# Kernel tuning notes

Hardware: AMD Instinct MI355X
Metric: run time of the kernel (lower is better)

Reference implementation:

```python
import jax, jax.numpy as jnp
import numpy as np

N_TOKENS = 16384
DIM = 1024
E = 8            # num_experts
K = 2            # top-k
CAP_FACTOR = 1.25


def setup_inputs() -> dict:
    key = jax.random.key(0)
    ks = jax.random.split(key, 4)
    sc = 0.02
    return {
        "x": jax.random.normal(ks[0], (N_TOKENS, DIM), jnp.float32),
        "Wr": jax.random.normal(ks[1], (E, DIM), jnp.float32) * sc,
        "br": jnp.zeros((E,), jnp.float32),
        "W1": jax.random.normal(ks[2], (E, DIM, DIM), jnp.float32) * sc,
        "b1": jnp.zeros((E, DIM), jnp.float32),
        "W2": jax.random.normal(ks[3], (E, DIM, DIM), jnp.float32) * sc,
        "b2": jnp.zeros((E, DIM), jnp.float32),
    }


def reference(x, Wr, br, W1, b1, W2, b2):
    N, D = x.shape
    capacity = int(CAP_FACTOR * N / E)  # static python int

    # --- NoisyTopKRouter (eval mode: no noise) ---
    logits = x @ Wr.T + br                                   # [N, E]
    topk_vals, topk_idx = jax.lax.top_k(logits, K)           # [N, K]
    gates_k = jax.nn.softmax(topk_vals, axis=-1)             # [N, K]
    sparse_gates = jnp.zeros_like(logits).at[
        jnp.arange(N)[:, None], topk_idx].set(gates_k)       # [N, E]

    # --- dispatch: first `capacity` tokens (in token order) per expert ---
    mask = sparse_gates > 0                                  # [N, E]
    # stable argsort puts routed tokens first, preserving token order
    order = jnp.argsort(jnp.logical_not(mask), axis=0, stable=True)[:capacity]  # [cap, E]
    valid = jnp.take_along_axis(mask, order, axis=0)         # [cap, E] bool

    tokens = x[order]                                        # [cap, E, D]
    h = jax.nn.relu(jnp.einsum('ced,eod->ceo', tokens, W1) + b1)  # [cap, E, D]
    expert_out = jnp.einsum('ceh,eoh->ceo', h, W2) + b2           # [cap, E, D]

    # --- combine: weight by gate, zero out padding, scatter-add back ---
    w = jnp.take_along_axis(sparse_gates, order, axis=0) * valid.astype(x.dtype)  # [cap, E]
    contrib = expert_out * w[..., None]                      # [cap, E, D]
    output = jnp.zeros_like(x).at[order.reshape(-1)].add(contrib.reshape(-1, D))

    # --- load-balancing stats ---
    load = valid.sum(axis=0).astype(x.dtype)                 # [E]
    load_dist = load / (load.sum() + 1e-8)
    load_loss = -(load_dist * jnp.log(load_dist + 1e-8)).sum()
    return output, load_loss, load_dist
```

## Files before the change

### kernel.cpp

```cpp
#include <hip/hip_runtime.h>
#include <hip/hip_bf16.h>
#include <cstdint>
#include <cstddef>

#define N_TOK   16384
#define DIM     1024
#define NE      8
#define CAP     2560
#define NCHUNK  256
#define NSLOT   (NE * CAP)

#define APL_BYTES  ((size_t)NSLOT * DIM * 2)
#define WPL_BYTES  ((size_t)NE * DIM * DIM * 2)
#define H_BYTES    ((size_t)NSLOT * DIM * 4)
#define TOK_BYTES  ((size_t)NSLOT * 4)
#define GATE_BYTES ((size_t)NSLOT * 4)
#define TIDX_BYTES ((size_t)N_TOK * 2 * 4)
#define TGT_BYTES  ((size_t)N_TOK * 2 * 4)
#define TSLOT_BYTES ((size_t)N_TOK * 2 * 4)
#define CC_BYTES   ((size_t)NE * NCHUNK * 4)
#define CO_BYTES   ((size_t)NE * NCHUNK * 4)
#define SMALL_BYTES (TOK_BYTES + GATE_BYTES + TIDX_BYTES + TGT_BYTES + TSLOT_BYTES + CC_BYTES + CO_BYTES)

typedef __attribute__((ext_vector_type(8))) short short8;
typedef __attribute__((ext_vector_type(4))) short short4v;
typedef __attribute__((ext_vector_type(4))) float floatx4;

__device__ __forceinline__ short f2bf(float f) {
    union { float f; unsigned u; } c; c.f = f;
    unsigned r = (c.u + 0x7fffu + ((c.u >> 16) & 1u)) >> 16;
    return (short)r;
}
__device__ __forceinline__ float bf2f(short s) {
    union { unsigned u; float f; } c; c.u = ((unsigned)(unsigned short)s) << 16;
    return c.f;
}

__device__ __forceinline__ void gload_lds16(const void* g, void* l) {
    typedef const __attribute__((address_space(1))) unsigned int* gp_t;
    typedef __attribute__((address_space(3))) unsigned int* lp_t;
    __builtin_amdgcn_global_load_lds((gp_t)g, (lp_t)l, 16, 0, 0);
}

__global__ __launch_bounds__(256) void router_kernel(
    const float* __restrict__ x, const float* __restrict__ Wr,
    const float* __restrict__ br, int* __restrict__ tokIdx,
    float* __restrict__ tokGate)
{
    int wave = threadIdx.x >> 6;
    int lane = threadIdx.x & 63;
    int t = blockIdx.x * 4 + wave;

    float acc[NE];
#pragma unroll
    for (int e = 0; e < NE; ++e) acc[e] = 0.f;

    const float4* xr = (const float4*)(x + (size_t)t * DIM);
#pragma unroll
    for (int j = 0; j < 4; ++j) {
        float4 xv = xr[j * 64 + lane];
#pragma unroll
        for (int e = 0; e < NE; ++e) {
            float4 wv = ((const float4*)(Wr + e * DIM))[j * 64 + lane];
            acc[e] = fmaf(xv.x, wv.x, acc[e]);
            acc[e] = fmaf(xv.y, wv.y, acc[e]);
            acc[e] = fmaf(xv.z, wv.z, acc[e]);
            acc[e] = fmaf(xv.w, wv.w, acc[e]);
        }
    }
#pragma unroll
    for (int e = 0; e < NE; ++e) {
        float v = acc[e];
#pragma unroll
        for (int off = 32; off > 0; off >>= 1) v += __shfl_xor(v, off, 64);
        acc[e] = v;
    }
    if (lane == 0) {
        float l[NE];
#pragma unroll
        for (int e = 0; e < NE; ++e) l[e] = acc[e] + br[e];
        int i0 = 0; float v0 = l[0];
#pragma unroll
        for (int e = 1; e < NE; ++e) if (l[e] > v0) { v0 = l[e]; i0 = e; }
        int i1 = -1; float v1 = -3.4e38f;
#pragma unroll
        for (int e = 0; e < NE; ++e) if (e != i0 && l[e] > v1) { v1 = l[e]; i1 = e; }
        float e1 = expf(v1 - v0);
        float g0 = 1.f / (1.f + e1);
        float g1 = e1 * g0;
        tokIdx[2 * t] = i0;  tokIdx[2 * t + 1] = i1;
        tokGate[2 * t] = g0; tokGate[2 * t + 1] = g1;
    }
}

__global__ __launch_bounds__(64) void count_kernel(
    const int* __restrict__ tokIdx, int* __restrict__ chunkCounts)
{
    int lane = threadIdx.x;
    int t = blockIdx.x * 64 + lane;
    int i0 = tokIdx[2 * t], i1 = tokIdx[2 * t + 1];
#pragma unroll
    for (int e = 0; e < NE; ++e) {
        unsigned long long m = __ballot(i0 == e || i1 == e);
        if (lane == 0) chunkCounts[e * NCHUNK + blockIdx.x] = __popcll(m);
    }
}

__global__ __launch_bounds__(256) void scan_kernel(
    const int* __restrict__ chunkCounts, int* __restrict__ chunkOffs,
    float* __restrict__ outTail)
{
    __shared__ int s[NCHUNK];
    __shared__ int totals[NE];
    int tid = threadIdx.x;
    for (int e = 0; e < NE; ++e) {
        int v = chunkCounts[e * NCHUNK + tid];
        s[tid] = v;
        __syncthreads();
        for (int off = 1; off < NCHUNK; off <<= 1) {
            int add = (tid >= off) ? s[tid - off] : 0;
            __syncthreads();
            s[tid] += add;
            __syncthreads();
        }
        chunkOffs[e * NCHUNK + tid] = s[tid] - v;
        if (tid == NCHUNK - 1) totals[e] = s[tid];
        __syncthreads();
    }
    if (tid == 0) {
        float load[NE]; float sum = 0.f;
        for (int e = 0; e < NE; ++e) {
            int c = totals[e]; if (c > CAP) c = CAP;
            load[e] = (float)c; sum += load[e];
        }
        float inv = 1.f / (sum + 1e-8f);
        float loss = 0.f;
        for (int e = 0; e < NE; ++e) {
            float d = load[e] * inv;
            loss -= d * logf(d + 1e-8f);
            outTail[1 + e] = d;
        }
        outTail[0] = loss;
    }
}

__global__ __launch_bounds__(64) void emit_kernel(
    const int* __restrict__ tokIdx, const float* __restrict__ tokGate,
    const int* __restrict__ chunkOffs, int* __restrict__ expTok,
    float* __restrict__ expGate, int* __restrict__ tokenSlot)
{
    int lane = threadIdx.x;
    int t = blockIdx.x * 64 + lane;
    int i0 = tokIdx[2 * t], i1 = tokIdx[2 * t + 1];
    float g0 = tokGate[2 * t], g1 = tokGate[2 * t + 1];
#pragma unroll
    for (int e = 0; e < NE; ++e) {
        bool r0 = (i0 == e), r1 = (i1 == e);
        unsigned long long m = __ballot(r0 || r1);
        if (r0 || r1) {
            int rank = chunkOffs[e * NCHUNK + blockIdx.x] +
                       __popcll(m & ((1ull << lane) - 1ull));
            int k = r0 ? 0 : 1;
            if (rank < CAP) {
                expTok[e * CAP + rank] = t;
                expGate[e * CAP + rank] = r0 ? g0 : g1;
                tokenSlot[2 * t + k] = e * CAP + rank;
            } else {
                tokenSlot[2 * t + k] = -1;
            }
        }
    }
}

__global__ __launch_bounds__(256) void convert_kernel(
    const float* __restrict__ src, short* __restrict__ hi,
    short* __restrict__ lo, int n4)
{
    int i = blockIdx.x * 256 + threadIdx.x;
    if (i >= n4) return;
    float4 v = ((const float4*)src)[i];
    short4v h, l;
    h.x = f2bf(v.x); h.y = f2bf(v.y); h.z = f2bf(v.z); h.w = f2bf(v.w);
    l.x = f2bf(v.x - bf2f(h.x)); l.y = f2bf(v.y - bf2f(h.y));
    l.z = f2bf(v.z - bf2f(h.z)); l.w = f2bf(v.w - bf2f(h.w));
    ((short4v*)hi)[i] = h;
    ((short4v*)lo)[i] = l;
}

__global__ __launch_bounds__(256) void gather_kernel(
    const float* __restrict__ x, const int* __restrict__ expTok,
    short* __restrict__ Ahi, short* __restrict__ Alo)
{
    int slot = blockIdx.x;
    int tok = expTok[slot];
    int c = threadIdx.x * 4;
    float4 v = *(const float4*)(x + (size_t)tok * DIM + c);
    short4v h, l;
    h.x = f2bf(v.x); h.y = f2bf(v.y); h.z = f2bf(v.z); h.w = f2bf(v.w);
    l.x = f2bf(v.x - bf2f(h.x)); l.y = f2bf(v.y - bf2f(h.y));
    l.z = f2bf(v.z - bf2f(h.z)); l.w = f2bf(v.w - bf2f(h.w));
    *(short4v*)(Ahi + (size_t)slot * DIM + c) = h;
    *(short4v*)(Alo + (size_t)slot * DIM + c) = l;
}


__device__ __forceinline__ void stage_tile(
    const short* __restrict__ aP, const short* __restrict__ bP,
    int rowBaseA, int rowBaseB, int k0,
    char* ldsA, char* ldsB, int wave, int lane)
{
    const int srow  = lane >> 3;
    const int xcol  = ((lane & 7) ^ srow) * 8;
    const short* ga = aP + (size_t)(rowBaseA + wave * 32 + srow) * DIM + k0 + xcol;
    const short* gb = bP + (size_t)(rowBaseB + wave * 32 + srow) * DIM + k0 + xcol;
    char* la = ldsA + (wave * 32) * 128;
    char* lb = ldsB + (wave * 32) * 128;
#pragma unroll
    for (int g = 0; g < 4; ++g)
        gload_lds16(ga + (size_t)(g * 8) * DIM, la + g * 1024);
#pragma unroll
    for (int g = 0; g < 4; ++g)
        gload_lds16(gb + (size_t)(g * 8) * DIM, lb + g * 1024);
}

template <int MODE>
__global__ __launch_bounds__(256) void mfma_gemm(
    const short* __restrict__ Ahi, const short* __restrict__ Alo,
    const short* __restrict__ Whi, const short* __restrict__ Wlo,
    const float* __restrict__ bias, const float* __restrict__ expGate,
    short* __restrict__ Ohi, short* __restrict__ Olo,
    float* __restrict__ EO)
{
    __shared__ __align__(16) char lds[65536];

    const int flat = blockIdx.x;
    const int swz  = (flat & 7) * 160 + (flat >> 3);
    const int e  = swz / 160;
    const int r  = swz % 160;
    const int tm = r >> 3;
    const int tn = r & 7;

    const int tid  = threadIdx.x;
    const int wave = tid >> 6;
    const int lane = tid & 63;
    const int wm = (wave >> 1) * 64;
    const int wn = (wave & 1) * 64;

    const int rowBaseA = e * CAP + tm * 128;
    const int rowBaseB = tn * 128;
    const short* Wh = Whi + (size_t)e * DIM * DIM;
    const short* Wl = Wlo + (size_t)e * DIM * DIM;

    const int frow = lane & 15;
    const int fq   = lane >> 4;

    floatx4 acc[4][4];
#pragma unroll
    for (int i = 0; i < 4; ++i)
#pragma unroll
        for (int j = 0; j < 4; ++j) acc[i][j] = (floatx4)0.f;

    stage_tile(Ahi, Wh, rowBaseA, rowBaseB, 0, lds, lds + 16384, wave, lane);
    __syncthreads();

#pragma unroll 2
    for (int t = 0; t < 48; ++t) {
        const int p = t & 1;
        char* bufA = lds + p * 32768;
        char* bufB = bufA + 16384;
        if (t < 47) {
            const int t1 = t + 1;
            const int seg = t1 >> 4;
            const int k0  = (t1 & 15) << 6;
            const short* aP = (seg == 2) ? Alo : Ahi;
            const short* bP = (seg == 1) ? Wl : Wh;
            stage_tile(aP, bP, rowBaseA, rowBaseB, k0,
                       lds + (p ^ 1) * 32768, lds + (p ^ 1) * 32768 + 16384,
                       wave, lane);
        }
#pragma unroll
        for (int kc = 0; kc < 2; ++kc) {
            const int bo = ((kc * 4 + fq) ^ (frow & 7)) * 16;
            short8 af[4], bf[4];
#pragma unroll
            for (int i = 0; i < 4; ++i)
                af[i] = *(const short8*)(bufA + (wm + i * 16 + frow) * 128 + bo);
#pragma unroll
            for (int j = 0; j < 4; ++j)
                bf[j] = *(const short8*)(bufB + (wn + j * 16 + frow) * 128 + bo);
            __builtin_amdgcn_s_setprio(1);
#pragma unroll
            for (int i = 0; i < 4; ++i)
#pragma unroll
                for (int j = 0; j < 4; ++j)
                    acc[i][j] = __builtin_amdgcn_mfma_f32_16x16x32_bf16(
                        af[i], bf[j], acc[i][j], 0, 0, 0);
            __builtin_amdgcn_s_setprio(0);
        }
        __syncthreads();
    }

    const int colBase = tn * 128 + wn;
#pragma unroll
    for (int j = 0; j < 4; ++j) {
        const int gc = colBase + j * 16 + (lane & 15);
        const float bj = bias[(size_t)e * DIM + gc];
#pragma unroll
        for (int i = 0; i < 4; ++i) {
            const int lr0 = wm + i * 16 + (lane >> 4) * 4;
#pragma unroll
            for (int rr = 0; rr < 4; ++rr) {
                const int lr = tm * 128 + lr0 + rr;
                float v = acc[i][j][rr] + bj;
                if (MODE == 0) {
                    v = fmaxf(v, 0.f);
                    short hi = f2bf(v);
                    short lo = f2bf(v - bf2f(hi));
                    size_t idx = (size_t)(e * CAP + lr) * DIM + gc;
                    Ohi[idx] = hi;
                    Olo[idx] = lo;
                } else {
                    float g = expGate[e * CAP + lr];
                    EO[(size_t)(e * CAP + lr) * DIM + gc] = v * g;
                }
            }
        }
    }
}

__global__ __launch_bounds__(256) void combine_kernel(
    const float* __restrict__ EO, const int* __restrict__ tokenSlot,
    float* __restrict__ out)
{
    int t = blockIdx.x;
    int col = threadIdx.x * 4;
    int p0 = tokenSlot[2 * t], p1 = tokenSlot[2 * t + 1];
    float4 s = make_float4(0.f, 0.f, 0.f, 0.f);
    if (p0 >= 0) {
        float4 v = *(const float4*)(EO + (size_t)p0 * DIM + col);
        s.x += v.x; s.y += v.y; s.z += v.z; s.w += v.w;
    }
    if (p1 >= 0) {
        float4 v = *(const float4*)(EO + (size_t)p1 * DIM + col);
        s.x += v.x; s.y += v.y; s.z += v.z; s.w += v.w;
    }
    *(float4*)(out + (size_t)t * DIM + col) = s;
}

#define BM 128
#define BN 128
#define BKF 8

__global__ __launch_bounds__(256) void f32gemm1_kernel(
    const float* __restrict__ x, const float* __restrict__ W1,
    const float* __restrict__ b1, const int* __restrict__ expTok,
    float* __restrict__ h)
{
    int e = blockIdx.z;
    int tm = blockIdx.x, tn = blockIdx.y;
    const float* W = W1 + (size_t)e * DIM * DIM;
    __shared__ float As[BKF][BM];
    __shared__ float Bs[BKF][BN];
    int tid = threadIdx.x;
    int lrow = tid >> 1, lk4 = (tid & 1) * 4;
    int rm = tid >> 4, rn = tid & 15;
    int tok = expTok[e * CAP + tm * BM + lrow];
    const float* aPtr = x + (size_t)tok * DIM + lk4;
    const float* bPtr = W + (size_t)(tn * BN + lrow) * DIM + lk4;
    float acc[8][8];
#pragma unroll
    for (int i = 0; i < 8; ++i)
#pragma unroll
        for (int j = 0; j < 8; ++j) acc[i][j] = 0.f;
    for (int k0 = 0; k0 < DIM; k0 += BKF) {
        float4 av = *(const float4*)(aPtr + k0);
        float4 bv = *(const float4*)(bPtr + k0);
        __syncthreads();
        As[lk4 + 0][lrow] = av.x; As[lk4 + 1][lrow] = av.y;
        As[lk4 + 2][lrow] = av.z; As[lk4 + 3][lrow] = av.w;
        Bs[lk4 + 0][lrow] = bv.x; Bs[lk4 + 1][lrow] = bv.y;
        Bs[lk4 + 2][lrow] = bv.z; Bs[lk4 + 3][lrow] = bv.w;
        __syncthreads();
#pragma unroll
        for (int k = 0; k < BKF; ++k) {
            float4 a0 = *(const float4*)&As[k][rm * 4];
            float4 a1 = *(const float4*)&As[k][64 + rm * 4];
            float4 b0 = *(const float4*)&Bs[k][rn * 4];
            float4 b1r = *(const float4*)&Bs[k][64 + rn * 4];
            float ar[8] = {a0.x,a0.y,a0.z,a0.w,a1.x,a1.y,a1.z,a1.w};
            float bc[8] = {b0.x,b0.y,b0.z,b0.w,b1r.x,b1r.y,b1r.z,b1r.w};
#pragma unroll
            for (int i = 0; i < 8; ++i)
#pragma unroll
                for (int j = 0; j < 8; ++j)
                    acc[i][j] = fmaf(ar[i], bc[j], acc[i][j]);
        }
    }
    int o0 = tn * BN + rn * 4;
    float4 blo = *(const float4*)(b1 + e * DIM + o0);
    float4 bhi = *(const float4*)(b1 + e * DIM + o0 + 64);
#pragma unroll
    for (int i = 0; i < 8; ++i) {
        int c = tm * BM + ((i < 4) ? (rm * 4 + i) : (64 + rm * 4 + i - 4));
        float* hr = h + ((size_t)e * CAP + c) * DIM;
        float4 lo = make_float4(fmaxf(acc[i][0] + blo.x, 0.f),
                                fmaxf(acc[i][1] + blo.y, 0.f),
                                fmaxf(acc[i][2] + blo.z, 0.f),
                                fmaxf(acc[i][3] + blo.w, 0.f));
        float4 hi = make_float4(fmaxf(acc[i][4] + bhi.x, 0.f),
                                fmaxf(acc[i][5] + bhi.y, 0.f),
                                fmaxf(acc[i][6] + bhi.z, 0.f),
                                fmaxf(acc[i][7] + bhi.w, 0.f));
        *(float4*)(hr + o0) = lo;
        *(float4*)(hr + o0 + 64) = hi;
    }
}

__global__ __launch_bounds__(256) void f32gemm2_kernel(
    const float* __restrict__ h, const float* __restrict__ W2,
    const float* __restrict__ b2, const int* __restrict__ expTok,
    const float* __restrict__ expGate, float* __restrict__ out)
{
    int e = blockIdx.z;
    int tm = blockIdx.x, tn = blockIdx.y;
    const float* W = W2 + (size_t)e * DIM * DIM;
    __shared__ float As[BKF][BM];
    __shared__ float Bs[BKF][BN];
    int tid = threadIdx.x;
    int lrow = tid >> 1, lk4 = (tid & 1) * 4;
    int rm = tid >> 4, rn = tid & 15;
    const float* aPtr = h + ((size_t)e * CAP + tm * BM + lrow) * DIM + lk4;
    const float* bPtr = W + (size_t)(tn * BN + lrow) * DIM + lk4;
    float acc[8][8];
#pragma unroll
    for (int i = 0; i < 8; ++i)
#pragma unroll
        for (int j = 0; j < 8; ++j) acc[i][j] = 0.f;
    for (int k0 = 0; k0 < DIM; k0 += BKF) {
        float4 av = *(const float4*)(aPtr + k0);
        float4 bv = *(const float4*)(bPtr + k0);
        __syncthreads();
        As[lk4 + 0][lrow] = av.x; As[lk4 + 1][lrow] = av.y;
        As[lk4 + 2][lrow] = av.z; As[lk4 + 3][lrow] = av.w;
        Bs[lk4 + 0][lrow] = bv.x; Bs[lk4 + 1][lrow] = bv.y;
        Bs[lk4 + 2][lrow] = bv.z; Bs[lk4 + 3][lrow] = bv.w;
        __syncthreads();
#pragma unroll
        for (int k = 0; k < BKF; ++k) {
            float4 a0 = *(const float4*)&As[k][rm * 4];
            float4 a1 = *(const float4*)&As[k][64 + rm * 4];
            float4 b0 = *(const float4*)&Bs[k][rn * 4];
            float4 b1r = *(const float4*)&Bs[k][64 + rn * 4];
            float ar[8] = {a0.x,a0.y,a0.z,a0.w,a1.x,a1.y,a1.z,a1.w};
            float bc[8] = {b0.x,b0.y,b0.z,b0.w,b1r.x,b1r.y,b1r.z,b1r.w};
#pragma unroll
            for (int i = 0; i < 8; ++i)
#pragma unroll
                for (int j = 0; j < 8; ++j)
                    acc[i][j] = fmaf(ar[i], bc[j], acc[i][j]);
        }
    }
    int o0 = tn * BN + rn * 4;
    float4 blo = *(const float4*)(b2 + e * DIM + o0);
    float4 bhi = *(const float4*)(b2 + e * DIM + o0 + 64);
#pragma unroll
    for (int i = 0; i < 8; ++i) {
        int c = tm * BM + ((i < 4) ? (rm * 4 + i) : (64 + rm * 4 + i - 4));
        float g = expGate[e * CAP + c];
        if (g != 0.f) {
            int t = expTok[e * CAP + c];
            float* orow = out + (size_t)t * DIM;
            atomicAdd(orow + o0 + 0, (acc[i][0] + blo.x) * g);
            atomicAdd(orow + o0 + 1, (acc[i][1] + blo.y) * g);
            atomicAdd(orow + o0 + 2, (acc[i][2] + blo.z) * g);
            atomicAdd(orow + o0 + 3, (acc[i][3] + blo.w) * g);
            atomicAdd(orow + o0 + 64, (acc[i][4] + bhi.x) * g);
            atomicAdd(orow + o0 + 65, (acc[i][5] + bhi.y) * g);
            atomicAdd(orow + o0 + 66, (acc[i][6] + bhi.z) * g);
            atomicAdd(orow + o0 + 67, (acc[i][7] + bhi.w) * g);
        }
    }
}

extern "C" void kernel_launch(void* const* d_in, const int* in_sizes, int n_in,
                              void* d_out, int out_size, void* d_ws, size_t ws_size,
                              hipStream_t stream)
{
    const float* x  = (const float*)d_in[0];
    const float* Wr = (const float*)d_in[1];
    const float* br = (const float*)d_in[2];
    const float* W1 = (const float*)d_in[3];
    const float* b1 = (const float*)d_in[4];
    const float* W2 = (const float*)d_in[5];
    const float* b2 = (const float*)d_in[6];
    float* out = (float*)d_out;

    char* ws = (char*)d_ws;
    const size_t needMfma = 4 * APL_BYTES + 4 * WPL_BYTES + SMALL_BYTES;

    if (ws_size >= needMfma) {
        size_t off = 0;
        short* Ahi = (short*)(ws + off); off += APL_BYTES;
        short* Alo = (short*)(ws + off); off += APL_BYTES;
        short* Hhi = (short*)(ws + off); off += APL_BYTES;
        short* Hlo = (short*)(ws + off); off += APL_BYTES;
        short* W1h = (short*)(ws + off); off += WPL_BYTES;
        short* W1l = (short*)(ws + off); off += WPL_BYTES;
        short* W2h = (short*)(ws + off); off += WPL_BYTES;
        short* W2l = (short*)(ws + off); off += WPL_BYTES;
        int*   expTok  = (int*)(ws + off);   off += TOK_BYTES;
        float* expGate = (float*)(ws + off); off += GATE_BYTES;
        int*   tokIdx  = (int*)(ws + off);   off += TIDX_BYTES;
        float* tokGate = (float*)(ws + off); off += TGT_BYTES;
        int*   tokenSlot = (int*)(ws + off); off += TSLOT_BYTES;
        int*   chunkCounts = (int*)(ws + off); off += CC_BYTES;
        int*   chunkOffs   = (int*)(ws + off); off += CO_BYTES;
        float* EO = (float*)Ahi;

        hipMemsetAsync(expTok, 0, TOK_BYTES + GATE_BYTES, stream);

        router_kernel<<<N_TOK / 4, 256, 0, stream>>>(x, Wr, br, tokIdx, tokGate);
        count_kernel<<<NCHUNK, 64, 0, stream>>>(tokIdx, chunkCounts);
        scan_kernel<<<1, 256, 0, stream>>>(chunkCounts, chunkOffs,
                                           out + (size_t)N_TOK * DIM);
        emit_kernel<<<NCHUNK, 64, 0, stream>>>(tokIdx, tokGate, chunkOffs,
                                               expTok, expGate, tokenSlot);

        const int wN4 = NE * DIM * DIM / 4;
        convert_kernel<<<wN4 / 256, 256, 0, stream>>>(W1, W1h, W1l, wN4);
        convert_kernel<<<wN4 / 256, 256, 0, stream>>>(W2, W2h, W2l, wN4);
        gather_kernel<<<NSLOT, 256, 0, stream>>>(x, expTok, Ahi, Alo);

        const int nblk = (NSLOT / 128) * (DIM / 128);
        mfma_gemm<0><<<nblk, 256, 0, stream>>>(Ahi, Alo, W1h, W1l, b1, nullptr,
                                               Hhi, Hlo, nullptr);
        mfma_gemm<1><<<nblk, 256, 0, stream>>>(Hhi, Hlo, W2h, W2l, b2, expGate,
                                               nullptr, nullptr, EO);
        combine_kernel<<<N_TOK, 256, 0, stream>>>(EO, tokenSlot, out);
    } else {
        size_t off = 0;
        float* h = (float*)(ws + off); off += H_BYTES;
        int*   expTok  = (int*)(ws + off);   off += TOK_BYTES;
        float* expGate = (float*)(ws + off); off += GATE_BYTES;
        int*   tokIdx  = (int*)(ws + off);   off += TIDX_BYTES;
        float* tokGate = (float*)(ws + off); off += TGT_BYTES;
        int*   tokenSlot = (int*)(ws + off); off += TSLOT_BYTES;
        int*   chunkCounts = (int*)(ws + off); off += CC_BYTES;
        int*   chunkOffs   = (int*)(ws + off); off += CO_BYTES;

        hipMemsetAsync(expTok, 0, TOK_BYTES + GATE_BYTES, stream);
        hipMemsetAsync(out, 0, (size_t)N_TOK * DIM * sizeof(float), stream);

        router_kernel<<<N_TOK / 4, 256, 0, stream>>>(x, Wr, br, tokIdx, tokGate);
        count_kernel<<<NCHUNK, 64, 0, stream>>>(tokIdx, chunkCounts);
        scan_kernel<<<1, 256, 0, stream>>>(chunkCounts, chunkOffs,
                                           out + (size_t)N_TOK * DIM);
        emit_kernel<<<NCHUNK, 64, 0, stream>>>(tokIdx, tokGate, chunkOffs,
                                               expTok, expGate, tokenSlot);

        dim3 gg(CAP / BM, DIM / BN, NE);
        f32gemm1_kernel<<<gg, 256, 0, stream>>>(x, W1, b1, expTok, h);
        f32gemm2_kernel<<<gg, 256, 0, stream>>>(h, W2, b2, expTok, expGate, out);
    }
}
```

Measured before the change: 517.4 us.

## Use wave-shuffle scan, fuse weight conversions, and fine-grain GEMM pipeline waits

The single-block scan now gives each of 8 waves one expert and uses shuffle-based prefix sums instead of an LDS scan with many block barriers. The two weight-conversion launches are merged into one kernel. In the MFMA GEMM main loop, the full __syncthreads is replaced by an explicit s_waitcnt vmcnt(8) plus raw s_barrier with sched_barriers, so the next tile's global loads can stay in flight while the current tile is computed. The vmcnt count depends on how many loads stage_tile issues, and if that assumption is wrong the loop could read incomplete LDS data.

```diff
diff --git a/kernel.cpp b/kernel.cpp
--- a/kernel.cpp
+++ b/kernel.cpp
@@ -106,28 +106,30 @@
     }
 }
 
-__global__ __launch_bounds__(256) void scan_kernel(
+__global__ __launch_bounds__(512) void scan_kernel(
     const int* __restrict__ chunkCounts, int* __restrict__ chunkOffs,
     float* __restrict__ outTail)
 {
-    __shared__ int s[NCHUNK];
     __shared__ int totals[NE];
-    int tid = threadIdx.x;
-    for (int e = 0; e < NE; ++e) {
-        int v = chunkCounts[e * NCHUNK + tid];
-        s[tid] = v;
-        __syncthreads();
-        for (int off = 1; off < NCHUNK; off <<= 1) {
-            int add = (tid >= off) ? s[tid - off] : 0;
-            __syncthreads();
-            s[tid] += add;
-            __syncthreads();
-        }
-        chunkOffs[e * NCHUNK + tid] = s[tid] - v;
-        if (tid == NCHUNK - 1) totals[e] = s[tid];
-        __syncthreads();
-    }
-    if (tid == 0) {
+    int wave = threadIdx.x >> 6;
+    int lane = threadIdx.x & 63;
+    int running = 0;
+#pragma unroll
+    for (int g = 0; g < 4; ++g) {
+        int idx = g * 64 + lane;
+        int v = chunkCounts[wave * NCHUNK + idx];
+        int s = v;
+#pragma unroll
+        for (int off = 1; off < 64; off <<= 1) {
+            int u = __shfl_up(s, off, 64);
+            if (lane >= off) s += u;
+        }
+        chunkOffs[wave * NCHUNK + idx] = running + s - v;
+        running += __shfl(s, 63, 64);
+    }
+    if (lane == 0) totals[wave] = running;
+    __syncthreads();
+    if (threadIdx.x == 0) {
         float load[NE]; float sum = 0.f;
         for (int e = 0; e < NE; ++e) {
             int c = totals[e]; if (c > CAP) c = CAP;
@@ -172,19 +174,22 @@
     }
 }
 
-__global__ __launch_bounds__(256) void convert_kernel(
-    const float* __restrict__ src, short* __restrict__ hi,
-    short* __restrict__ lo, int n4)
+__global__ __launch_bounds__(256) void convert2_kernel(
+    const float* __restrict__ W1, const float* __restrict__ W2,
+    short* __restrict__ W1h, short* __restrict__ W1l,
+    short* __restrict__ W2h, short* __restrict__ W2l, int n4each)
 {
     int i = blockIdx.x * 256 + threadIdx.x;
-    if (i >= n4) return;
-    float4 v = ((const float4*)src)[i];
+    const float* src; short* hi; short* lo; int k;
+    if (i < n4each) { src = W1; hi = W1h; lo = W1l; k = i; }
+    else            { src = W2; hi = W2h; lo = W2l; k = i - n4each; }
+    float4 v = ((const float4*)src)[k];
     short4v h, l;
     h.x = f2bf(v.x); h.y = f2bf(v.y); h.z = f2bf(v.z); h.w = f2bf(v.w);
     l.x = f2bf(v.x - bf2f(h.x)); l.y = f2bf(v.y - bf2f(h.y));
     l.z = f2bf(v.z - bf2f(h.z)); l.w = f2bf(v.w - bf2f(h.w));
-    ((short4v*)hi)[i] = h;
-    ((short4v*)lo)[i] = l;
+    ((short4v*)hi)[k] = h;
+    ((short4v*)lo)[k] = l;
 }
 
 __global__ __launch_bounds__(256) void gather_kernel(
@@ -261,23 +266,27 @@
         for (int j = 0; j < 4; ++j) acc[i][j] = (floatx4)0.f;
 
     stage_tile(Ahi, Wh, rowBaseA, rowBaseB, 0, lds, lds + 16384, wave, lane);
-    __syncthreads();
-
-#pragma unroll 2
+
+#pragma unroll 1
     for (int t = 0; t < 48; ++t) {
-        const int p = t & 1;
-        char* bufA = lds + p * 32768;
+        char* bufA = lds + (t & 1) * 32768;
         char* bufB = bufA + 16384;
-        if (t < 47) {
-            const int t1 = t + 1;
+        const int t1 = t + 1;
+        if (t1 < 48) {
             const int seg = t1 >> 4;
             const int k0  = (t1 & 15) << 6;
             const short* aP = (seg == 2) ? Alo : Ahi;
             const short* bP = (seg == 1) ? Wl : Wh;
-            stage_tile(aP, bP, rowBaseA, rowBaseB, k0,
-                       lds + (p ^ 1) * 32768, lds + (p ^ 1) * 32768 + 16384,
+            char* dstA = lds + (t1 & 1) * 32768;
+            stage_tile(aP, bP, rowBaseA, rowBaseB, k0, dstA, dstA + 16384,
                        wave, lane);
-        }
+            asm volatile("s_waitcnt vmcnt(8)" ::: "memory");
+        } else {
+            asm volatile("s_waitcnt vmcnt(0)" ::: "memory");
+        }
+        __builtin_amdgcn_sched_barrier(0);
+        __builtin_amdgcn_s_barrier();
+        __builtin_amdgcn_sched_barrier(0);
 #pragma unroll
         for (int kc = 0; kc < 2; ++kc) {
             const int bo = ((kc * 4 + fq) ^ (frow & 7)) * 16;
@@ -297,7 +306,8 @@
                         af[i], bf[j], acc[i][j], 0, 0, 0);
             __builtin_amdgcn_s_setprio(0);
         }
-        __syncthreads();
+        __builtin_amdgcn_sched_barrier(0);
+        __builtin_amdgcn_s_barrier();
     }
 
     const int colBase = tn * 128 + wn;
@@ -521,14 +531,14 @@
 
         router_kernel<<<N_TOK / 4, 256, 0, stream>>>(x, Wr, br, tokIdx, tokGate);
         count_kernel<<<NCHUNK, 64, 0, stream>>>(tokIdx, chunkCounts);
-        scan_kernel<<<1, 256, 0, stream>>>(chunkCounts, chunkOffs,
+        scan_kernel<<<1, 512, 0, stream>>>(chunkCounts, chunkOffs,
                                            out + (size_t)N_TOK * DIM);
         emit_kernel<<<NCHUNK, 64, 0, stream>>>(tokIdx, tokGate, chunkOffs,
                                                expTok, expGate, tokenSlot);
 
         const int wN4 = NE * DIM * DIM / 4;
-        convert_kernel<<<wN4 / 256, 256, 0, stream>>>(W1, W1h, W1l, wN4);
-        convert_kernel<<<wN4 / 256, 256, 0, stream>>>(W2, W2h, W2l, wN4);
+        convert2_kernel<<<2 * wN4 / 256, 256, 0, stream>>>(W1, W2, W1h, W1l,
+                                                           W2h, W2l, wN4);
         gather_kernel<<<NSLOT, 256, 0, stream>>>(x, expTok, Ahi, Alo);
 
         const int nblk = (NSLOT / 128) * (DIM / 128);
@@ -553,7 +563,7 @@
 
         router_kernel<<<N_TOK / 4, 256, 0, stream>>>(x, Wr, br, tokIdx, tokGate);
         count_kernel<<<NCHUNK, 64, 0, stream>>>(tokIdx, chunkCounts);
-        scan_kernel<<<1, 256, 0, stream>>>(chunkCounts, chunkOffs,
+        scan_kernel<<<1, 512, 0, stream>>>(chunkCounts, chunkOffs,
                                            out + (size_t)N_TOK * DIM);
         emit_kernel<<<NCHUNK, 64, 0, stream>>>(tokIdx, tokGate, chunkOffs,
                                                expTok, expGate, tokenSlot);
```

Result: faster. 505.9 us (-2.2%).
